# Optimization experiments

Measured on AMD Instinct MI355X. Metric: run time of the kernel, lower is better.

The kernel has to match this reference:

```python
import jax, jax.numpy as jnp
import numpy as np
from jax import lax

B, T, V, LAT, U, P = 256, 128, 42, 200, 512, 3  # batch, seq, vocab, latent, lstm units, num_prop


def setup_inputs() -> dict:
    key = jax.random.key(0)
    ks = jax.random.split(key, 40)
    g = lambda i, shape, s=0.05: (jax.random.normal(ks[i], shape, jnp.float32) * s)
    inp = {
        'X': jax.random.randint(ks[0], (B, T), 0, V, jnp.int64 if jax.config.jax_enable_x64 else jnp.int32),
        'Y': jax.random.randint(ks[1], (B, T), 0, V, jnp.int32),
        'C': jax.random.normal(ks[2], (B, P), jnp.float32),
        'L': jax.random.randint(ks[3], (B,), 1, T + 1, jnp.int32),
        'eps': jax.random.normal(ks[4], (B, LAT), jnp.float32),
        'emb_enc': g(5, (V, LAT), 0.1),
        'emb_dec': g(6, (V, LAT), 0.1),
        # encoder stacked LSTM: layer0 input dim = LAT + P, layers 1-2 input dim = U
        'enc_k0': g(7, (LAT + P, 4 * U)), 'enc_rk0': g(8, (U, 4 * U)), 'enc_b0': jnp.zeros((4 * U,), jnp.float32),
        'enc_k1': g(9, (U, 4 * U)), 'enc_rk1': g(10, (U, 4 * U)), 'enc_b1': jnp.zeros((4 * U,), jnp.float32),
        'enc_k2': g(11, (U, 4 * U)), 'enc_rk2': g(12, (U, 4 * U)), 'enc_b2': jnp.zeros((4 * U,), jnp.float32),
        # decoder stacked LSTM: layer0 input dim = 2*LAT + P
        'dec_k0': g(13, (2 * LAT + P, 4 * U)), 'dec_rk0': g(14, (U, 4 * U)), 'dec_b0': jnp.zeros((4 * U,), jnp.float32),
        'dec_k1': g(15, (U, 4 * U)), 'dec_rk1': g(16, (U, 4 * U)), 'dec_b1': jnp.zeros((4 * U,), jnp.float32),
        'dec_k2': g(17, (U, 4 * U)), 'dec_rk2': g(18, (U, 4 * U)), 'dec_b2': jnp.zeros((4 * U,), jnp.float32),
        'Wm': g(19, (U, LAT)), 'bm': jnp.zeros((LAT,), jnp.float32),
        'Ws': g(20, (U, LAT)), 'bs': jnp.zeros((LAT,), jnp.float32),
        'Wo': g(21, (U, V)), 'bo': jnp.zeros((V,), jnp.float32),
    }
    return inp


def _lstm_step(x, h, c, k, rk, b):
    # Keras LSTMCell gate order: i, f, g(candidate), o
    z = x @ k + h @ rk + b
    i, f, gg, o = jnp.split(z, 4, axis=-1)
    c2 = jax.nn.sigmoid(f) * c + jax.nn.sigmoid(i) * jnp.tanh(gg)
    h2 = jax.nn.sigmoid(o) * jnp.tanh(c2)
    return h2, c2


def _run_stacked(inp, params):
    # inp: [B, T, D]; params: list of 3 (kernel, recurrent_kernel, bias)
    b = inp.shape[0]
    init = tuple((jnp.zeros((b, U), inp.dtype), jnp.zeros((b, U), inp.dtype)) for _ in range(3))

    def scan_fn(carry, x_t):
        h_in = x_t
        new = []
        for (h, c), (k, rk, bb) in zip(carry, params):
            h2, c2 = _lstm_step(h_in, h, c, k, rk, bb)
            new.append((h2, c2))
            h_in = h2
        return tuple(new), h_in

    carry, ys = lax.scan(scan_fn, init, jnp.swapaxes(inp, 0, 1))
    return jnp.swapaxes(ys, 0, 1), carry  # [B,T,U], final states


def reference(X, Y, C, L, eps, emb_enc, emb_dec,
              enc_k0, enc_rk0, enc_b0, enc_k1, enc_rk1, enc_b1, enc_k2, enc_rk2, enc_b2,
              dec_k0, dec_rk0, dec_b0, dec_k1, dec_rk1, dec_b1, dec_k2, dec_rk2, dec_b2,
              Wm, bm, Ws, bs, Wo, bo):
    enc_params = [(enc_k0, enc_rk0, enc_b0), (enc_k1, enc_rk1, enc_b1), (enc_k2, enc_rk2, enc_b2)]
    dec_params = [(dec_k0, dec_rk0, dec_b0), (dec_k1, dec_rk1, dec_b1), (dec_k2, dec_rk2, dec_b2)]

    # ---- encode ----
    Xe = emb_enc[X]                                       # [B,T,LAT]
    Ct = jnp.broadcast_to(C[:, None, :], (B, T, P))
    enc_in = jnp.concatenate([Xe, Ct], axis=-1)           # [B,T,LAT+P]
    _, enc_states = _run_stacked(enc_in, enc_params)
    h = enc_states[-1][1]                                 # CELL state of last layer (state[-1][1])
    mean = h @ Wm + bm
    log_sigma = h @ Ws + bs
    z = mean + jnp.exp(log_sigma / 2.0) * eps             # [B,LAT]

    # ---- decode ----
    Zt = jnp.broadcast_to(z[:, None, :], (B, T, LAT))
    Xd = emb_dec[X]
    dec_in = jnp.concatenate([Zt, Xd, Ct], axis=-1)       # [B,T,2*LAT+P]
    dec_out, _ = _run_stacked(dec_in, dec_params)
    pre = dec_out @ Wo + bo                               # pre-softmax logits [B,T,V]

    # ---- losses ----
    logp = jax.nn.log_softmax(pre, axis=-1)
    ce = -jnp.take_along_axis(logp, Y[..., None].astype(jnp.int32), axis=-1)[..., 0]  # [B,T]
    weights = (jnp.arange(T)[None, :] < L[:, None]).astype(jnp.float32)
    recon = jnp.mean(ce * weights)
    latent = -0.5 * jnp.mean(1.0 + log_sigma - jnp.square(mean) - jnp.exp(log_sigma))
    loss = recon + latent
    return loss, recon, latent
```

## Files before the change

### kernel.cpp

```cpp
#include <hip/hip_runtime.h>

#define B_ 256
#define T_ 128
#define V_ 42
#define LAT_ 200
#define U_ 512
#define G4_ 2048
#define NBLK 196
#define FI(r, m) ((((r) * 2) + (m)) * 32)
#define SLOT_ ((size_t)B_ * U_)
#define LS_ ((size_t)129 * SLOT_)

typedef unsigned short ushort_t;
typedef __attribute__((ext_vector_type(8))) short bf8;
typedef __attribute__((ext_vector_type(4))) float f4;

__device__ __forceinline__ ushort_t f2bf(float f) {
  union { float f; unsigned int i; } v; v.f = f;
  unsigned int r = v.i + 0x7fffu + ((v.i >> 16) & 1u);
  return (ushort_t)(r >> 16);
}
__device__ __forceinline__ float sigf(float x) { return 1.f / (1.f + __expf(-x)); }
__device__ __forceinline__ float tanhfast(float x) {
  float e = __expf(2.f * x);
  return 1.f - 2.f / (e + 1.f);
}
__device__ __forceinline__ void wait_vm0() {
  asm volatile("s_waitcnt vmcnt(0)" ::: "memory");
}
__device__ __forceinline__ void st_wt_b16(void* p, ushort_t v) {
  unsigned int vv = v;
  asm volatile("global_store_short %0, %1, off sc0 sc1" :: "v"(p), "v"(vv) : "memory");
}
__device__ __forceinline__ void st_wt_b32(void* p, unsigned int v) {
  asm volatile("global_store_dword %0, %1, off sc0 sc1" :: "v"(p), "v"(v) : "memory");
}

__global__ __launch_bounds__(256) void table_kernel(const float* emb, const float* k0, int roff, float* table) {
  int v = blockIdx.x, tid = threadIdx.x;
  __shared__ float e[LAT_];
  for (int i = tid; i < LAT_; i += 256) e[i] = emb[v * LAT_ + i];
  __syncthreads();
  for (int j = tid; j < G4_; j += 256) {
    float s = 0.f;
    for (int n = 0; n < LAT_; n++) s += e[n] * k0[(size_t)(roff + n) * G4_ + j];
    table[v * G4_ + j] = s;
  }
}

__device__ __forceinline__ size_t mat_off_u4(int m) {
  if (m == 0) return 0;
  if (m == 1) return 147456;
  if (m < 10) return 360448 + (size_t)(m - 2) * 131072;
  return 1409024;
}

struct SwzSrc {
  const float *enc_rk0, *enc_k0, *enc_b0;
  const float *dec_rk0, *dec_k0, *dec_b0;
  const float *tabE, *tabD;
  const float *encK1, *encR1, *encK2, *encR2;
  const float *decK1, *decR1, *decK2, *decR2;
  const float *Wo;
  ushort_t* dst;
};

__device__ float swz_val(const SwzSrc& s, int mat, int k, int n) {
  switch (mat) {
    case 0: {
      if (k < 512) return s.enc_rk0[(size_t)k * G4_ + n];
      int i = k - 512;
      if (i < 42) return s.tabE[(size_t)i * G4_ + n];
      if (i < 45) return s.enc_k0[(size_t)(200 + i - 42) * G4_ + n];
      if (i == 45) return s.enc_b0[n];
      return 0.f;
    }
    case 1: {
      if (k < 512) return s.dec_rk0[(size_t)k * G4_ + n];
      int i = k - 512;
      if (i < 200) return s.dec_k0[(size_t)i * G4_ + n];
      if (i < 256) return 0.f;
      i -= 256;
      if (i < 42) return s.tabD[(size_t)i * G4_ + n];
      if (i < 45) return s.dec_k0[(size_t)(400 + i - 42) * G4_ + n];
      if (i == 45) return s.dec_b0[n];
      return 0.f;
    }
    case 2: return s.encK1[(size_t)k * G4_ + n];
    case 3: return s.encR1[(size_t)k * G4_ + n];
    case 4: return s.encK2[(size_t)k * G4_ + n];
    case 5: return s.encR2[(size_t)k * G4_ + n];
    case 6: return s.decK1[(size_t)k * G4_ + n];
    case 7: return s.decR1[(size_t)k * G4_ + n];
    case 8: return s.decK2[(size_t)k * G4_ + n];
    case 9: return s.decR2[(size_t)k * G4_ + n];
    default: return (n < V_) ? s.Wo[(size_t)k * V_ + n] : 0.f;
  }
}

__global__ __launch_bounds__(256) void swz_ext_kernel(SwzSrc s) {
  int b = blockIdx.x, tid = threadIdx.x;
  int mat, nt16;
  if (b < 1280) { mat = b >> 7; nt16 = b & 127; } else { mat = 10; nt16 = b - 1280; }
  int ktMax = (mat == 0) ? 18 : (mat == 1) ? 26 : 16;
  int lane = tid & 63, l15 = lane & 15, q = lane >> 4;
  int n = nt16 * 16 + l15;
  uint4* dst = (uint4*)s.dst;
  size_t off = mat_off_u4(mat);
  for (int kt = tid >> 6; kt < ktMax; kt += 4) {
    ushort_t o[8];
    int kb = kt * 32 + q * 8;
#pragma unroll
    for (int j = 0; j < 8; j++) o[j] = f2bf(swz_val(s, mat, kb + j, n));
    dst[off + ((size_t)nt16 * ktMax + kt) * 64 + lane] = *(const uint4*)o;
  }
}

struct PP {
  const ushort_t* swz;
  ushort_t* ring;
  float* c2g; ushort_t* zf16; float* sums; int* bar; int* gen; int* flg; float* out;
  const float *enc_b1, *enc_b2, *dec_b1, *dec_b2;
  const float *Wm, *bm, *Ws, *bs, *eps, *C, *bo;
  const int *X, *Y, *Lb;
};

__device__ __forceinline__ void grid_barrier(int* bar, int* gen) {
  __builtin_amdgcn_fence(__ATOMIC_RELEASE, "agent");
  __syncthreads();
  if (threadIdx.x == 0) {
    int g = __hip_atomic_load(gen, __ATOMIC_RELAXED, __HIP_MEMORY_SCOPE_AGENT);
    if (__hip_atomic_fetch_add(bar, 1, __ATOMIC_ACQ_REL, __HIP_MEMORY_SCOPE_AGENT) == NBLK - 1) {
      __hip_atomic_store(bar, 0, __ATOMIC_RELAXED, __HIP_MEMORY_SCOPE_AGENT);
      __hip_atomic_store(gen, g + 1, __ATOMIC_RELEASE, __HIP_MEMORY_SCOPE_AGENT);
    } else {
      int gg;
      do {
        __builtin_amdgcn_s_sleep(1);
        gg = __hip_atomic_load(gen, __ATOMIC_ACQUIRE, __HIP_MEMORY_SCOPE_AGENT);
      } while (gg == g);
    }
  }
  __syncthreads();
  __builtin_amdgcn_fence(__ATOMIC_ACQUIRE, "agent");
}

#define MFMA(a, bfrag, c) __builtin_amdgcn_mfma_f32_16x16x32_bf16((a), (bfrag), (c), 0, 0, 0)

__device__ __forceinline__ void wait_flags(const int* f, int cnt, int target, f4* junk, bf8 ja) {
  int lane = threadIdx.x & 63;
  const int* a = f + (lane < cnt ? lane : 0);
  for (;;) {
    int v = __hip_atomic_load(a, __ATOMIC_RELAXED, __HIP_MEMORY_SCOPE_AGENT);
    bool bad = (lane < cnt) && (v < target);
    if (__ballot(bad) == 0ull) return;
#pragma unroll
    for (int i = 0; i < 8; i++) *junk = MFMA(ja, ja, *junk);
  }
}

__global__ __launch_bounds__(256, 1) void persist(PP p) {
  __shared__ uint4 wlds4[8192];
  const int b = blockIdx.x, tid = threadIdx.x;
  const int lane = tid & 63, w = tid >> 6, q = lane >> 4, l15 = lane & 15;
  const int role = b < 64 ? 0 : b < 128 ? 1 : b < 192 ? 2 : 3;
  const int idx = b & 63;
  const int ut = idx >> 1;
  const int mi = idx & 1;
  const int m0 = mi * 128;
  const int rw = m0 + w * 32;
  const int u = ut * 16 + l15;
  const uint4* swzU4 = (const uint4*)p.swz;
  const int cb = b - 192;

  unsigned char* tok = (unsigned char*)wlds4 + 106496;
  unsigned char* ytok = (unsigned char*)wlds4 + 49152;

  f4 junk = {0.f, 0.f, 0.f, 0.f};
  bf8 ja = {0, 0, 0, 0, 0, 0, 0, 0};

  ushort_t cb0[2][3];
  if (role == 0) {
#pragma unroll
    for (int ms = 0; ms < 2; ms++)
#pragma unroll
      for (int j = 0; j < 3; j++) cb0[ms][j] = f2bf(p.C[(rw + ms * 16 + l15) * 3 + j]);
  }

  const int pubidx = FI(role, mi) + ut;

  float ce_local = 0.f;
  float boR0 = 0.f, boR1 = 0.f, boR2 = 0.f;
  int Lr[4] = {0, 0, 0, 0};
  int pub = 0;

  for (int phase = 0; phase < 2; phase++) {
    const bool dec = (phase == 1);

    if (dec) {
      grid_barrier(p.bar, p.gen);
      if (b < 50) {
        int lat0 = b * 4;
        int row = tid;
        float m[4], ls[4];
#pragma unroll
        for (int lc = 0; lc < 4; lc++) { m[lc] = p.bm[lat0 + lc]; ls[lc] = p.bs[lat0 + lc]; }
        const float* cr = p.c2g + (size_t)row * U_;
        for (int k = 0; k < U_; k++) {
          float hv = cr[k];
#pragma unroll
          for (int lc = 0; lc < 4; lc++) {
            m[lc] += hv * p.Wm[k * LAT_ + lat0 + lc];
            ls[lc] += hv * p.Ws[k * LAT_ + lat0 + lc];
          }
        }
        float kl = 0.f;
#pragma unroll
        for (int lc = 0; lc < 4; lc++) {
          int lat = lat0 + lc;
          float zz = m[lc] + __expf(0.5f * ls[lc]) * p.eps[row * LAT_ + lat];
          p.zf16[row * 256 + lat] = f2bf(zz);
          kl += 1.f + ls[lc] - m[lc] * m[lc] - __expf(ls[lc]);
        }
        float* red = (float*)wlds4;
        red[tid] = kl; __syncthreads();
        for (int st = 128; st > 0; st >>= 1) { if (tid < st) red[tid] += red[tid + st]; __syncthreads(); }
        if (tid == 0) atomicAdd(p.sums + 1, red[0]);
      }
      __syncthreads();
    }

    if (role == 0) {
      if (!dec) {
        size_t mo = mat_off_u4(0);
        for (int g = 0; g < 4; g++) {
          int nt16 = g * 32 + ut;
          size_t src = mo + (size_t)nt16 * 18 * 64;
          int dst = g * 18 * 64;
          for (int i = tid; i < 18 * 64; i += 256) wlds4[dst + i] = swzU4[src + i];
        }
        for (int i = tid; i < 128 * T_; i += 256) {
          int r = i >> 7, t = i & 127;
          tok[r * 133 + t] = (unsigned char)p.X[(size_t)(m0 + r) * T_ + t];
        }
      } else {
        size_t mo = mat_off_u4(1);
        for (int g = 0; g < 4; g++) {
          int nt16 = g * 32 + ut;
          size_t src = mo + (size_t)nt16 * 26 * 64;
          int dst = g * 18 * 64;
          for (int i = tid; i < 16 * 64; i += 256) wlds4[dst + i] = swzU4[src + i];
          for (int i = tid; i < 2 * 64; i += 256) wlds4[dst + 16 * 64 + i] = swzU4[src + 24 * 64 + i];
          for (int i = tid; i < 8 * 64; i += 256) wlds4[4608 + g * 512 + i] = swzU4[src + 16 * 64 + i];
        }
      }
    } else if (role <= 2) {
      int matK = dec ? (role == 1 ? 6 : 8) : (role == 1 ? 2 : 4);
      for (int gm = 0; gm < 2; gm++) {
        size_t mo = mat_off_u4(matK + gm);
        for (int g = 0; g < 4; g++) {
          int nt16 = g * 32 + ut;
          size_t src = mo + (size_t)nt16 * 1024;
          int dst = gm * 4096 + g * 1024;
          for (int i = tid; i < 1024; i += 256) wlds4[dst + i] = swzU4[src + i];
        }
      }
    } else if (dec) {
      size_t mo = mat_off_u4(10);
      for (int i = tid; i < 3072; i += 256) wlds4[i] = swzU4[mo + i];
      for (int i = tid; i < 64 * T_; i += 256) {
        int r = i >> 7, t = i & 127;
        ytok[r * 133 + t] = (unsigned char)p.Y[(size_t)(cb * 64 + r) * T_ + t];
      }
      int r0c = cb * 64 + w * 16;
      boR0 = p.bo[l15]; boR1 = p.bo[16 + l15]; boR2 = (l15 < 10) ? p.bo[32 + l15] : 0.f;
#pragma unroll
      for (int r = 0; r < 4; r++) Lr[r] = p.Lb[r0c + q * 4 + r];
    }
    __syncthreads();

    float creg[2][4];
#pragma unroll
    for (int ms = 0; ms < 2; ms++)
#pragma unroll
      for (int r = 0; r < 4; r++) creg[ms][r] = 0.f;
    float bias[4] = {0.f, 0.f, 0.f, 0.f};
    if (role == 1 || role == 2) {
      const float* bb = dec ? (role == 1 ? p.dec_b1 : p.dec_b2) : (role == 1 ? p.enc_b1 : p.enc_b2);
#pragma unroll
      for (int g = 0; g < 4; g++) bias[g] = bb[g * 512 + u];
    }

    const int* myp = nullptr; int myc = 0;
    if (role == 0) {
      if (w == 0) { myp = p.flg + FI(0, mi); myc = 32; }
    } else if (role == 1) {
      if (w == 0) { myp = p.flg + FI(0, mi); myc = 32; }
      else if (w == 1) { myp = p.flg + FI(1, mi); myc = 32; }
    } else if (role == 2) {
      if (w == 0) { myp = p.flg + FI(1, mi); myc = 32; }
      else if (w == 1) { myp = p.flg + FI(2, mi); myc = 32; }
    } else {
      if (w == 0) { myp = p.flg + FI(2, cb >> 1); myc = 32; }
    }

    grid_barrier(p.bar, p.gen);

    f4 zacc[2][4];
#pragma unroll
    for (int ms = 0; ms < 2; ms++)
#pragma unroll
      for (int g = 0; g < 4; g++) zacc[ms][g] = (f4){0.f, 0.f, 0.f, 0.f};
    if (role == 0 && dec) {
      const ushort_t* Az0 = p.zf16 + (rw + l15) * 256 + q * 8;
#pragma unroll
      for (int kz = 0; kz < 8; kz++) {
        bf8 a0 = *(const bf8*)(Az0 + kz * 32);
        bf8 a1 = *(const bf8*)(Az0 + 16 * 256 + kz * 32);
#pragma unroll
        for (int g = 0; g < 4; g++) {
          bf8 bbf = *(const bf8*)&wlds4[4608 + g * 512 + kz * 64 + lane];
          zacc[0][g] = MFMA(a0, bbf, zacc[0][g]);
          zacc[1][g] = MFMA(a1, bbf, zacc[1][g]);
        }
      }
    }

    const int smax = dec ? T_ + 3 : T_ + 2;
    for (int s = 0; s < smax; s++) {
      pub++;
      if (myc) wait_flags(myp, myc, pub - 1, &junk, ja);
      __syncthreads();

      const int lag = (role <= 2) ? role : 3;
      const int t = s - lag;
      if (role == 3) {
        if (dec && t >= 0 && t < T_) {
          int r0c = cb * 64 + w * 16;
          const ushort_t* Ar = p.ring + 2 * LS_ + (size_t)(t + 1) * SLOT_ + (size_t)(r0c + l15) * U_ + q * 8;
          f4 a3[3];
#pragma unroll
          for (int nt = 0; nt < 3; nt++) a3[nt] = (f4){0.f, 0.f, 0.f, 0.f};
#pragma unroll 4
          for (int kt = 0; kt < 16; kt++) {
            bf8 a = *(const bf8*)(Ar + kt * 32);
#pragma unroll
            for (int nt = 0; nt < 3; nt++) {
              bf8 bbf = *(const bf8*)&wlds4[nt * 1024 + kt * 64 + lane];
              a3[nt] = MFMA(a, bbf, a3[nt]);
            }
          }
#pragma unroll
          for (int r = 0; r < 4; r++) {
            float v0 = a3[0][r] + boR0;
            float v1 = a3[1][r] + boR1;
            float v2 = (l15 < 10) ? a3[2][r] + boR2 : -3.0e38f;
            float mx = fmaxf(fmaxf(v0, v1), v2);
            mx = fmaxf(mx, __shfl_xor(mx, 1)); mx = fmaxf(mx, __shfl_xor(mx, 2));
            mx = fmaxf(mx, __shfl_xor(mx, 4)); mx = fmaxf(mx, __shfl_xor(mx, 8));
            float se = __expf(v0 - mx) + __expf(v1 - mx) + ((l15 < 10) ? __expf(v2 - mx) : 0.f);
            int yv = ytok[(w * 16 + q * 4 + r) * 133 + t];
            float py = (l15 == yv ? v0 : 0.f) + (l15 + 16 == yv ? v1 : 0.f) + (l15 + 32 == yv ? v2 : 0.f);
            se += __shfl_xor(se, 1); se += __shfl_xor(se, 2); se += __shfl_xor(se, 4); se += __shfl_xor(se, 8);
            py += __shfl_xor(py, 1); py += __shfl_xor(py, 2); py += __shfl_xor(py, 4); py += __shfl_xor(py, 8);
            if (l15 == 0 && t < Lr[r]) ce_local += mx + __logf(se) - py;
          }
        }
      } else if (t >= 0 && t < T_) {
        f4 acc[2][4];
#pragma unroll
        for (int ms = 0; ms < 2; ms++)
#pragma unroll
          for (int g = 0; g < 4; g++) acc[ms][g] = zacc[ms][g];

        const ushort_t* hin = p.ring + (size_t)role * LS_ + (size_t)t * SLOT_;
        ushort_t* hout = p.ring + (size_t)role * LS_ + (size_t)(t + 1) * SLOT_;
        const ushort_t* Ah0 = hin + (size_t)(rw + l15) * U_ + q * 8;
        const ushort_t* Ah1 = Ah0 + 16 * U_;

        if (role == 0) {
          const int KT64 = 18 * 64;
#pragma unroll 4
          for (int kt = 0; kt < 16; kt++) {
            bf8 a0 = *(const bf8*)(Ah0 + kt * 32);
            bf8 a1 = *(const bf8*)(Ah1 + kt * 32);
#pragma unroll
            for (int g = 0; g < 4; g++) {
              bf8 bbf = *(const bf8*)&wlds4[g * KT64 + kt * 64 + lane];
              acc[0][g] = MFMA(a0, bbf, acc[0][g]);
              acc[1][g] = MFMA(a1, bbf, acc[1][g]);
            }
          }
          int xv0 = tok[(w * 32 + l15) * 133 + t];
          int xv1 = tok[(w * 32 + 16 + l15) * 133 + t];
#pragma unroll
          for (int ktc = 0; ktc < 2; ktc++) {
            union { ushort_t us[8]; bf8 v; } a0u, a1u;
#pragma unroll
            for (int j = 0; j < 8; j++) {
              int id = ktc * 32 + q * 8 + j;
              ushort_t v0 = (id == xv0) ? (ushort_t)0x3F80 : (ushort_t)0;
              ushort_t v1 = (id == xv1) ? (ushort_t)0x3F80 : (ushort_t)0;
              if (id >= 42 && id < 45) { v0 = cb0[0][id - 42]; v1 = cb0[1][id - 42]; }
              if (id == 45) { v0 = 0x3F80; v1 = 0x3F80; }
              a0u.us[j] = v0; a1u.us[j] = v1;
            }
            int kt = 16 + ktc;
#pragma unroll
            for (int g = 0; g < 4; g++) {
              bf8 bbf = *(const bf8*)&wlds4[g * KT64 + kt * 64 + lane];
              acc[0][g] = MFMA(a0u.v, bbf, acc[0][g]);
              acc[1][g] = MFMA(a1u.v, bbf, acc[1][g]);
            }
          }
        } else {
          const ushort_t* xin = p.ring + (size_t)(role - 1) * LS_ + (size_t)(t + 1) * SLOT_;
          const ushort_t* Ax0 = xin + (size_t)(rw + l15) * U_ + q * 8;
          const ushort_t* Ax1 = Ax0 + 16 * U_;
#pragma unroll 4
          for (int kt = 0; kt < 16; kt++) {
            bf8 a0 = *(const bf8*)(Ax0 + kt * 32);
            bf8 a1 = *(const bf8*)(Ax1 + kt * 32);
#pragma unroll
            for (int g = 0; g < 4; g++) {
              bf8 bbf = *(const bf8*)&wlds4[g * 1024 + kt * 64 + lane];
              acc[0][g] = MFMA(a0, bbf, acc[0][g]);
              acc[1][g] = MFMA(a1, bbf, acc[1][g]);
            }
          }
#pragma unroll 4
          for (int kt = 0; kt < 16; kt++) {
            bf8 a0 = *(const bf8*)(Ah0 + kt * 32);
            bf8 a1 = *(const bf8*)(Ah1 + kt * 32);
#pragma unroll
            for (int g = 0; g < 4; g++) {
              bf8 bbf = *(const bf8*)&wlds4[4096 + g * 1024 + kt * 64 + lane];
              acc[0][g] = MFMA(a0, bbf, acc[0][g]);
              acc[1][g] = MFMA(a1, bbf, acc[1][g]);
            }
          }
        }

#pragma unroll
        for (int ms = 0; ms < 2; ms++)
#pragma unroll
          for (int r = 0; r < 4; r++) {
            int row = rw + ms * 16 + q * 4 + r;
            float zi = acc[ms][0][r] + bias[0];
            float zf = acc[ms][1][r] + bias[1];
            float zg = acc[ms][2][r] + bias[2];
            float zo = acc[ms][3][r] + bias[3];
            float cp = creg[ms][r];
            float cn = sigf(zf) * cp + sigf(zi) * tanhfast(zg);
            float hn = sigf(zo) * tanhfast(cn);
            creg[ms][r] = cn;
            st_wt_b16(&hout[(size_t)row * U_ + u], f2bf(hn));
            if (!dec && role == 2 && t == T_ - 1) p.c2g[(size_t)row * U_ + u] = cn;
          }
      }
      wait_vm0();
      __syncthreads();
      if (tid == 0 && role < 3) st_wt_b32(p.flg + pubidx, (unsigned int)pub);
    }
  }

  if (p.X[0] == 0x12345678 && tid == 0) atomicAdd(p.out, junk[0]);

  if (role == 3 && l15 == 0) atomicAdd(p.sums + 0, ce_local);
  grid_barrier(p.bar, p.gen);
  if (b == 0 && tid == 0) {
    float recon = p.sums[0] * (1.f / ((float)B_ * (float)T_));
    float latent = -0.5f * p.sums[1] * (1.f / ((float)B_ * (float)LAT_));
    p.out[0] = recon + latent;
    p.out[1] = recon;
    p.out[2] = latent;
  }
}

extern "C" void kernel_launch(void* const* d_in, const int* in_sizes, int n_in,
                              void* d_out, int out_size, void* d_ws, size_t ws_size,
                              hipStream_t stream) {
  const int*   X       = (const int*)d_in[0];
  const int*   Y       = (const int*)d_in[1];
  const float* C       = (const float*)d_in[2];
  const int*   L       = (const int*)d_in[3];
  const float* eps     = (const float*)d_in[4];
  const float* emb_enc = (const float*)d_in[5];
  const float* emb_dec = (const float*)d_in[6];
  const float* enc_k0  = (const float*)d_in[7];
  const float* enc_rk0 = (const float*)d_in[8];
  const float* enc_b0  = (const float*)d_in[9];
  const float* enc_k1  = (const float*)d_in[10];
  const float* enc_rk1 = (const float*)d_in[11];
  const float* enc_b1  = (const float*)d_in[12];
  const float* enc_k2  = (const float*)d_in[13];
  const float* enc_rk2 = (const float*)d_in[14];
  const float* enc_b2  = (const float*)d_in[15];
  const float* dec_k0  = (const float*)d_in[16];
  const float* dec_rk0 = (const float*)d_in[17];
  const float* dec_b0  = (const float*)d_in[18];
  const float* dec_k1  = (const float*)d_in[19];
  const float* dec_rk1 = (const float*)d_in[20];
  const float* dec_b1  = (const float*)d_in[21];
  const float* dec_k2  = (const float*)d_in[22];
  const float* dec_rk2 = (const float*)d_in[23];
  const float* dec_b2  = (const float*)d_in[24];
  const float* Wm      = (const float*)d_in[25];
  const float* bm      = (const float*)d_in[26];
  const float* Ws      = (const float*)d_in[27];
  const float* bs      = (const float*)d_in[28];
  const float* Wo      = (const float*)d_in[29];
  const float* bo      = (const float*)d_in[30];
  float* out = (float*)d_out;
  (void)in_sizes; (void)n_in; (void)out_size; (void)ws_size;

  char* wsb = (char*)d_ws;
  size_t o = 0;
  auto take = [&](size_t bytes) -> char* { char* p = wsb + o; o += (bytes + 255) & ~(size_t)255; return p; };

  float* c2g  = (float*)take((size_t)B_ * U_ * 4);
  ushort_t* zf16 = (ushort_t*)take((size_t)B_ * 256 * 2);
  float* sums = (float*)take(8);
  int* bar = (int*)take(4);
  int* gen = (int*)take(4);
  int* flg = (int*)take(4 * 2 * 32 * 4);
  size_t zero_bytes = o;
  ushort_t* ring = (ushort_t*)take(3 * LS_ * 2);
  ushort_t* swz = (ushort_t*)take((size_t)1412096 * 16);
  float* tabE = (float*)take((size_t)V_ * G4_ * 4);
  float* tabD = (float*)take((size_t)V_ * G4_ * 4);

  hipMemsetAsync(wsb, 0, zero_bytes, stream);
  for (int l = 0; l < 3; l++)
    hipMemsetAsync(ring + (size_t)l * LS_, 0, SLOT_ * 2, stream);

  table_kernel<<<V_, 256, 0, stream>>>(emb_enc, enc_k0, 0, tabE);
  table_kernel<<<V_, 256, 0, stream>>>(emb_dec, dec_k0, 200, tabD);

  SwzSrc ss;
  ss.enc_rk0 = enc_rk0; ss.enc_k0 = enc_k0; ss.enc_b0 = enc_b0;
  ss.dec_rk0 = dec_rk0; ss.dec_k0 = dec_k0; ss.dec_b0 = dec_b0;
  ss.tabE = tabE; ss.tabD = tabD;
  ss.encK1 = enc_k1; ss.encR1 = enc_rk1; ss.encK2 = enc_k2; ss.encR2 = enc_rk2;
  ss.decK1 = dec_k1; ss.decR1 = dec_rk1; ss.decK2 = dec_k2; ss.decR2 = dec_rk2;
  ss.Wo = Wo; ss.dst = swz;
  swz_ext_kernel<<<1283, 256, 0, stream>>>(ss);

  PP pp;
  pp.swz = swz; pp.ring = ring;
  pp.c2g = c2g; pp.zf16 = zf16; pp.sums = sums; pp.bar = bar; pp.gen = gen; pp.flg = flg; pp.out = out;
  pp.enc_b1 = enc_b1; pp.enc_b2 = enc_b2; pp.dec_b1 = dec_b1; pp.dec_b2 = dec_b2;
  pp.Wm = Wm; pp.bm = bm; pp.Ws = Ws; pp.bs = bs; pp.eps = eps; pp.C = C; pp.bo = bo;
  pp.X = X; pp.Y = Y; pp.Lb = L;
  persist<<<NBLK, 256, 0, stream>>>(pp);
}
```

Baseline: 4.997 ms.

## Pack h stores into 64-bit writes and add MFMA busy-work to hold clocks

Each LSTM hidden-state output was written as a separate 16-bit write-through store. Lanes now exchange bf16 values through two xor shuffles so that one lane in four issues a single 8-byte write-through store, cutting the store count on the critical cross-block handoff. The flag-wait loop and the end of each step now run dummy MFMA chains across four independent accumulators, apparently to keep the matrix units busy and the clocks high while spinning. The dummy work costs power and adds latency to every step, and its effect depends on the device's clock behaviour.

Result: slower. 6.057 ms (+21.2%).

```diff
diff --git a/kernel.cpp b/kernel.cpp
--- a/kernel.cpp
+++ b/kernel.cpp
@@ -28,12 +28,11 @@
 __device__ __forceinline__ void wait_vm0() {
   asm volatile("s_waitcnt vmcnt(0)" ::: "memory");
 }
-__device__ __forceinline__ void st_wt_b16(void* p, ushort_t v) {
-  unsigned int vv = v;
-  asm volatile("global_store_short %0, %1, off sc0 sc1" :: "v"(p), "v"(vv) : "memory");
-}
 __device__ __forceinline__ void st_wt_b32(void* p, unsigned int v) {
   asm volatile("global_store_dword %0, %1, off sc0 sc1" :: "v"(p), "v"(v) : "memory");
+}
+__device__ __forceinline__ void st_wt_b64(void* p, unsigned long long v) {
+  asm volatile("global_store_dwordx2 %0, %1, off sc0 sc1" :: "v"(p), "v"(v) : "memory");
 }
 
 __global__ __launch_bounds__(256) void table_kernel(const float* emb, const float* k0, int roff, float* table) {
@@ -147,15 +146,19 @@
 
 #define MFMA(a, bfrag, c) __builtin_amdgcn_mfma_f32_16x16x32_bf16((a), (bfrag), (c), 0, 0, 0)
 
-__device__ __forceinline__ void wait_flags(const int* f, int cnt, int target, f4* junk, bf8 ja) {
+__device__ __forceinline__ void wait_flags(const int* f, int cnt, int target, f4* jk, bf8 ja) {
   int lane = threadIdx.x & 63;
   const int* a = f + (lane < cnt ? lane : 0);
+  int burn = 0;
   for (;;) {
     int v = __hip_atomic_load(a, __ATOMIC_RELAXED, __HIP_MEMORY_SCOPE_AGENT);
+    for (int i = 0; i < burn; i++) {
+      jk[0] = MFMA(ja, ja, jk[0]); jk[1] = MFMA(ja, ja, jk[1]);
+      jk[2] = MFMA(ja, ja, jk[2]); jk[3] = MFMA(ja, ja, jk[3]);
+    }
     bool bad = (lane < cnt) && (v < target);
     if (__ballot(bad) == 0ull) return;
-#pragma unroll
-    for (int i = 0; i < 8; i++) *junk = MFMA(ja, ja, *junk);
+    burn = 32;
   }
 }
 
@@ -176,7 +179,7 @@
   unsigned char* tok = (unsigned char*)wlds4 + 106496;
   unsigned char* ytok = (unsigned char*)wlds4 + 49152;
 
-  f4 junk = {0.f, 0.f, 0.f, 0.f};
+  f4 junk[4] = {{0.f,0.f,0.f,0.f},{0.f,0.f,0.f,0.f},{0.f,0.f,0.f,0.f},{0.f,0.f,0.f,0.f}};
   bf8 ja = {0, 0, 0, 0, 0, 0, 0, 0};
 
   ushort_t cb0[2][3];
@@ -329,7 +332,7 @@
     const int smax = dec ? T_ + 3 : T_ + 2;
     for (int s = 0; s < smax; s++) {
       pub++;
-      if (myc) wait_flags(myp, myc, pub - 1, &junk, ja);
+      if (myc) wait_flags(myp, myc, pub - 1, junk, ja);
       __syncthreads();
 
       const int lag = (role <= 2) ? role : 3;
@@ -454,9 +457,22 @@
             float cn = sigf(zf) * cp + sigf(zi) * tanhfast(zg);
             float hn = sigf(zo) * tanhfast(cn);
             creg[ms][r] = cn;
-            st_wt_b16(&hout[(size_t)row * U_ + u], f2bf(hn));
+            unsigned int v0 = (unsigned int)f2bf(hn);
+            unsigned int pr = (unsigned int)__shfl_xor((int)v0, 1);
+            unsigned int p2 = (l15 & 1) ? ((pr & 0xffffu) | (v0 << 16))
+                                        : ((v0 & 0xffffu) | (pr << 16));
+            unsigned int pr2 = (unsigned int)__shfl_xor((int)p2, 2);
+            unsigned long long p4 = (l15 & 2)
+              ? (((unsigned long long)pr2) | (((unsigned long long)p2) << 32))
+              : (((unsigned long long)p2) | (((unsigned long long)pr2) << 32));
+            if ((l15 & 3) == 0)
+              st_wt_b64(&hout[(size_t)row * U_ + ut * 16 + (l15 & 12)], p4);
             if (!dec && role == 2 && t == T_ - 1) p.c2g[(size_t)row * U_ + u] = cn;
           }
+      }
+      for (int i = 0; i < 16; i++) {
+        junk[0] = MFMA(ja, ja, junk[0]); junk[1] = MFMA(ja, ja, junk[1]);
+        junk[2] = MFMA(ja, ja, junk[2]); junk[3] = MFMA(ja, ja, junk[3]);
       }
       wait_vm0();
       __syncthreads();
@@ -464,7 +480,8 @@
     }
   }
 
-  if (p.X[0] == 0x12345678 && tid == 0) atomicAdd(p.out, junk[0]);
+  if (p.X[0] == 0x12345678 && tid == 0)
+    atomicAdd(p.out, junk[0][0] + junk[1][0] + junk[2][0] + junk[3][0]);
 
   if (role == 3 && l15 == 0) atomicAdd(p.sums + 0, ce_local);
   grid_barrier(p.bar, p.gen);
```

## Prefetch layer inputs one step ahead and remap blocks across 256 CUs

Applied to the files above, without the earlier changes.

Blocks are remapped so roles interleave across the grid (grp = b&7), and the grid grows to 256 blocks, with extra idle/projection blocks. Layers 1–2 and the output head now load next step's input activations into registers (xpre/arpre) after computing the current step, waiting on the upstream flag early, and the pipeline lag doubles to allow this. The MFMA-spinning junk loop in wait_flags is removed. This trades register pressure and more pipeline stages for hiding global-load latency behind the recurrence.

New measurement: 9.215 ms. +84.4%, slower.

```diff
diff --git a/kernel.cpp b/kernel.cpp
--- a/kernel.cpp
+++ b/kernel.cpp
@@ -6,7 +6,7 @@
 #define LAT_ 200
 #define U_ 512
 #define G4_ 2048
-#define NBLK 196
+#define NBLK 256
 #define FI(r, m) ((((r) * 2) + (m)) * 32)
 #define SLOT_ ((size_t)B_ * U_)
 #define LS_ ((size_t)129 * SLOT_)
@@ -145,39 +145,36 @@
   __builtin_amdgcn_fence(__ATOMIC_ACQUIRE, "agent");
 }
 
-#define MFMA(a, bfrag, c) __builtin_amdgcn_mfma_f32_16x16x32_bf16((a), (bfrag), (c), 0, 0, 0)
-
-__device__ __forceinline__ void wait_flags(const int* f, int cnt, int target, f4* junk, bf8 ja) {
+__device__ __forceinline__ void wait_flags(const int* f, int cnt, int target) {
   int lane = threadIdx.x & 63;
   const int* a = f + (lane < cnt ? lane : 0);
-  for (;;) {
+  bool bad;
+  do {
     int v = __hip_atomic_load(a, __ATOMIC_RELAXED, __HIP_MEMORY_SCOPE_AGENT);
-    bool bad = (lane < cnt) && (v < target);
-    if (__ballot(bad) == 0ull) return;
-#pragma unroll
-    for (int i = 0; i < 8; i++) *junk = MFMA(ja, ja, *junk);
-  }
-}
+    bad = (lane < cnt) && (v < target);
+  } while (__ballot(bad) != 0ull);
+}
+
+#define MFMA(a, bfrag, c) __builtin_amdgcn_mfma_f32_16x16x32_bf16((a), (bfrag), (c), 0, 0, 0)
 
 __global__ __launch_bounds__(256, 1) void persist(PP p) {
   __shared__ uint4 wlds4[8192];
   const int b = blockIdx.x, tid = threadIdx.x;
   const int lane = tid & 63, w = tid >> 6, q = lane >> 4, l15 = lane & 15;
-  const int role = b < 64 ? 0 : b < 128 ? 1 : b < 192 ? 2 : 3;
-  const int idx = b & 63;
-  const int ut = idx >> 1;
-  const int mi = idx & 1;
+
+  const int grp = b & 7, rank = b >> 3;
+  int role, mi = 0, cb = 0, pid = -1;
+  if (grp < 6) { role = grp >> 1; mi = grp & 1; }
+  else if (grp == 6 && rank < 4) { role = 3; cb = rank; mi = rank >> 1; }
+  else { role = 4; pid = (grp == 6) ? rank - 4 : 28 + rank; }
+  const int ut = rank;
   const int m0 = mi * 128;
   const int rw = m0 + w * 32;
   const int u = ut * 16 + l15;
   const uint4* swzU4 = (const uint4*)p.swz;
-  const int cb = b - 192;
 
   unsigned char* tok = (unsigned char*)wlds4 + 106496;
   unsigned char* ytok = (unsigned char*)wlds4 + 49152;
-
-  f4 junk = {0.f, 0.f, 0.f, 0.f};
-  bf8 ja = {0, 0, 0, 0, 0, 0, 0, 0};
 
   ushort_t cb0[2][3];
   if (role == 0) {
@@ -192,15 +189,15 @@
   float ce_local = 0.f;
   float boR0 = 0.f, boR1 = 0.f, boR2 = 0.f;
   int Lr[4] = {0, 0, 0, 0};
-  int pub = 0;
 
   for (int phase = 0; phase < 2; phase++) {
     const bool dec = (phase == 1);
+    const int base = dec ? (T_ + 4) : 0;
 
     if (dec) {
       grid_barrier(p.bar, p.gen);
-      if (b < 50) {
-        int lat0 = b * 4;
+      if (pid >= 0 && pid < 50) {
+        int lat0 = pid * 4;
         int row = tid;
         float m[4], ls[4];
 #pragma unroll
@@ -265,7 +262,7 @@
           for (int i = tid; i < 1024; i += 256) wlds4[dst + i] = swzU4[src + i];
         }
       }
-    } else if (dec) {
+    } else if (role == 3 && dec) {
       size_t mo = mat_off_u4(10);
       for (int i = tid; i < 3072; i += 256) wlds4[i] = swzU4[mo + i];
       for (int i = tid; i < 64 * T_; i += 256) {
@@ -291,19 +288,6 @@
       for (int g = 0; g < 4; g++) bias[g] = bb[g * 512 + u];
     }
 
-    const int* myp = nullptr; int myc = 0;
-    if (role == 0) {
-      if (w == 0) { myp = p.flg + FI(0, mi); myc = 32; }
-    } else if (role == 1) {
-      if (w == 0) { myp = p.flg + FI(0, mi); myc = 32; }
-      else if (w == 1) { myp = p.flg + FI(1, mi); myc = 32; }
-    } else if (role == 2) {
-      if (w == 0) { myp = p.flg + FI(1, mi); myc = 32; }
-      else if (w == 1) { myp = p.flg + FI(2, mi); myc = 32; }
-    } else {
-      if (w == 0) { myp = p.flg + FI(2, cb >> 1); myc = 32; }
-    }
-
     grid_barrier(p.bar, p.gen);
 
     f4 zacc[2][4];
@@ -326,145 +310,162 @@
       }
     }
 
-    const int smax = dec ? T_ + 3 : T_ + 2;
-    for (int s = 0; s < smax; s++) {
-      pub++;
-      if (myc) wait_flags(myp, myc, pub - 1, &junk, ja);
-      __syncthreads();
-
-      const int lag = (role <= 2) ? role : 3;
-      const int t = s - lag;
-      if (role == 3) {
-        if (dec && t >= 0 && t < T_) {
+    const bool active = (role < 3) || (role == 3 && dec);
+    if (active) {
+      const int lag = (role <= 2) ? 2 * role : 6;
+      const int smax = dec ? T_ + 6 : T_ + 4;
+      bf8 xpre[2][16];
+      bf8 arpre[16];
+      for (int s = 0; s < smax; s++) {
+        const int pubv = base + s + 1;
+        if (role < 3 && w == 0) wait_flags(p.flg + FI(role, mi), 32, pubv - 1);
+        __syncthreads();
+
+        const int t = s - lag;
+        if (role == 3) {
+          if (t >= 0 && t < T_) {
+            f4 a3[3];
+#pragma unroll
+            for (int nt = 0; nt < 3; nt++) a3[nt] = (f4){0.f, 0.f, 0.f, 0.f};
+#pragma unroll
+            for (int kt = 0; kt < 16; kt++) {
+#pragma unroll
+              for (int nt = 0; nt < 3; nt++) {
+                bf8 bbf = *(const bf8*)&wlds4[nt * 1024 + kt * 64 + lane];
+                a3[nt] = MFMA(arpre[kt], bbf, a3[nt]);
+              }
+            }
+#pragma unroll
+            for (int r = 0; r < 4; r++) {
+              float v0 = a3[0][r] + boR0;
+              float v1 = a3[1][r] + boR1;
+              float v2 = (l15 < 10) ? a3[2][r] + boR2 : -3.0e38f;
+              float mx = fmaxf(fmaxf(v0, v1), v2);
+              mx = fmaxf(mx, __shfl_xor(mx, 1)); mx = fmaxf(mx, __shfl_xor(mx, 2));
+              mx = fmaxf(mx, __shfl_xor(mx, 4)); mx = fmaxf(mx, __shfl_xor(mx, 8));
+              float se = __expf(v0 - mx) + __expf(v1 - mx) + ((l15 < 10) ? __expf(v2 - mx) : 0.f);
+              int yv = ytok[(w * 16 + q * 4 + r) * 133 + t];
+              float py = (l15 == yv ? v0 : 0.f) + (l15 + 16 == yv ? v1 : 0.f) + (l15 + 32 == yv ? v2 : 0.f);
+              se += __shfl_xor(se, 1); se += __shfl_xor(se, 2); se += __shfl_xor(se, 4); se += __shfl_xor(se, 8);
+              py += __shfl_xor(py, 1); py += __shfl_xor(py, 2); py += __shfl_xor(py, 4); py += __shfl_xor(py, 8);
+              if (l15 == 0 && t < Lr[r]) ce_local += mx + __logf(se) - py;
+            }
+          }
+        } else if (t >= 0 && t < T_) {
+          f4 acc[2][4];
+#pragma unroll
+          for (int ms = 0; ms < 2; ms++)
+#pragma unroll
+            for (int g = 0; g < 4; g++) acc[ms][g] = zacc[ms][g];
+
+          const ushort_t* hin = p.ring + (size_t)role * LS_ + (size_t)t * SLOT_;
+          ushort_t* hout = p.ring + (size_t)role * LS_ + (size_t)(t + 1) * SLOT_;
+          const ushort_t* Ah0 = hin + (size_t)(rw + l15) * U_ + q * 8;
+          const ushort_t* Ah1 = Ah0 + 16 * U_;
+
+          if (role == 0) {
+            const int KT64 = 18 * 64;
+#pragma unroll 4
+            for (int kt = 0; kt < 16; kt++) {
+              bf8 a0 = *(const bf8*)(Ah0 + kt * 32);
+              bf8 a1 = *(const bf8*)(Ah1 + kt * 32);
+#pragma unroll
+              for (int g = 0; g < 4; g++) {
+                bf8 bbf = *(const bf8*)&wlds4[g * KT64 + kt * 64 + lane];
+                acc[0][g] = MFMA(a0, bbf, acc[0][g]);
+                acc[1][g] = MFMA(a1, bbf, acc[1][g]);
+              }
+            }
+            int xv0 = tok[(w * 32 + l15) * 133 + t];
+            int xv1 = tok[(w * 32 + 16 + l15) * 133 + t];
+#pragma unroll
+            for (int ktc = 0; ktc < 2; ktc++) {
+              union { ushort_t us[8]; bf8 v; } a0u, a1u;
+#pragma unroll
+              for (int j = 0; j < 8; j++) {
+                int id = ktc * 32 + q * 8 + j;
+                ushort_t v0 = (id == xv0) ? (ushort_t)0x3F80 : (ushort_t)0;
+                ushort_t v1 = (id == xv1) ? (ushort_t)0x3F80 : (ushort_t)0;
+                if (id >= 42 && id < 45) { v0 = cb0[0][id - 42]; v1 = cb0[1][id - 42]; }
+                if (id == 45) { v0 = 0x3F80; v1 = 0x3F80; }
+                a0u.us[j] = v0; a1u.us[j] = v1;
+              }
+              int kt = 16 + ktc;
+#pragma unroll
+              for (int g = 0; g < 4; g++) {
+                bf8 bbf = *(const bf8*)&wlds4[g * KT64 + kt * 64 + lane];
+                acc[0][g] = MFMA(a0u.v, bbf, acc[0][g]);
+                acc[1][g] = MFMA(a1u.v, bbf, acc[1][g]);
+              }
+            }
+          } else {
+#pragma unroll
+            for (int kt = 0; kt < 16; kt++) {
+#pragma unroll
+              for (int g = 0; g < 4; g++) {
+                bf8 bbf = *(const bf8*)&wlds4[g * 1024 + kt * 64 + lane];
+                acc[0][g] = MFMA(xpre[0][kt], bbf, acc[0][g]);
+                acc[1][g] = MFMA(xpre[1][kt], bbf, acc[1][g]);
+              }
+            }
+#pragma unroll 4
+            for (int kt = 0; kt < 16; kt++) {
+              bf8 a0 = *(const bf8*)(Ah0 + kt * 32);
+              bf8 a1 = *(const bf8*)(Ah1 + kt * 32);
+#pragma unroll
+              for (int g = 0; g < 4; g++) {
+                bf8 bbf = *(const bf8*)&wlds4[4096 + g * 1024 + kt * 64 + lane];
+                acc[0][g] = MFMA(a0, bbf, acc[0][g]);
+                acc[1][g] = MFMA(a1, bbf, acc[1][g]);
+              }
+            }
+          }
+
+#pragma unroll
+          for (int ms = 0; ms < 2; ms++)
+#pragma unroll
+            for (int r = 0; r < 4; r++) {
+              int row = rw + ms * 16 + q * 4 + r;
+              float zi = acc[ms][0][r] + bias[0];
+              float zf = acc[ms][1][r] + bias[1];
+              float zg = acc[ms][2][r] + bias[2];
+              float zo = acc[ms][3][r] + bias[3];
+              float cp = creg[ms][r];
+              float cn = sigf(zf) * cp + sigf(zi) * tanhfast(zg);
+              float hn = sigf(zo) * tanhfast(cn);
+              creg[ms][r] = cn;
+              ushort_t hv = f2bf(hn);
+              ushort_t* addr = &hout[(size_t)row * U_ + u];
+              *addr = hv;
+              st_wt_b16(addr, hv);
+              if (!dec && role == 2 && t == T_ - 1) p.c2g[(size_t)row * U_ + u] = cn;
+            }
+        }
+
+        const int tn = s + 1 - lag;
+        if ((role == 1 || role == 2) && tn >= 0 && tn < T_) {
+          wait_flags(p.flg + FI(role - 1, mi), 32, pubv - 1);
+          const ushort_t* xin = p.ring + (size_t)(role - 1) * LS_ + (size_t)(tn + 1) * SLOT_;
+          const ushort_t* Ax0 = xin + (size_t)(rw + l15) * U_ + q * 8;
+#pragma unroll
+          for (int kt = 0; kt < 16; kt++) {
+            xpre[0][kt] = *(const bf8*)(Ax0 + kt * 32);
+            xpre[1][kt] = *(const bf8*)(Ax0 + 16 * U_ + kt * 32);
+          }
+        } else if (role == 3 && tn >= 0 && tn < T_) {
+          wait_flags(p.flg + FI(2, cb >> 1), 32, pubv - 1);
           int r0c = cb * 64 + w * 16;
-          const ushort_t* Ar = p.ring + 2 * LS_ + (size_t)(t + 1) * SLOT_ + (size_t)(r0c + l15) * U_ + q * 8;
-          f4 a3[3];
-#pragma unroll
-          for (int nt = 0; nt < 3; nt++) a3[nt] = (f4){0.f, 0.f, 0.f, 0.f};
-#pragma unroll 4
-          for (int kt = 0; kt < 16; kt++) {
-            bf8 a = *(const bf8*)(Ar + kt * 32);
-#pragma unroll
-            for (int nt = 0; nt < 3; nt++) {
-              bf8 bbf = *(const bf8*)&wlds4[nt * 1024 + kt * 64 + lane];
-              a3[nt] = MFMA(a, bbf, a3[nt]);
-            }
-          }
-#pragma unroll
-          for (int r = 0; r < 4; r++) {
-            float v0 = a3[0][r] + boR0;
-            float v1 = a3[1][r] + boR1;
-            float v2 = (l15 < 10) ? a3[2][r] + boR2 : -3.0e38f;
-            float mx = fmaxf(fmaxf(v0, v1), v2);
-            mx = fmaxf(mx, __shfl_xor(mx, 1)); mx = fmaxf(mx, __shfl_xor(mx, 2));
-            mx = fmaxf(mx, __shfl_xor(mx, 4)); mx = fmaxf(mx, __shfl_xor(mx, 8));
-            float se = __expf(v0 - mx) + __expf(v1 - mx) + ((l15 < 10) ? __expf(v2 - mx) : 0.f);
-            int yv = ytok[(w * 16 + q * 4 + r) * 133 + t];
-            float py = (l15 == yv ? v0 : 0.f) + (l15 + 16 == yv ? v1 : 0.f) + (l15 + 32 == yv ? v2 : 0.f);
-            se += __shfl_xor(se, 1); se += __shfl_xor(se, 2); se += __shfl_xor(se, 4); se += __shfl_xor(se, 8);
-            py += __shfl_xor(py, 1); py += __shfl_xor(py, 2); py += __shfl_xor(py, 4); py += __shfl_xor(py, 8);
-            if (l15 == 0 && t < Lr[r]) ce_local += mx + __logf(se) - py;
-          }
-        }
-      } else if (t >= 0 && t < T_) {
-        f4 acc[2][4];
-#pragma unroll
-        for (int ms = 0; ms < 2; ms++)
-#pragma unroll
-          for (int g = 0; g < 4; g++) acc[ms][g] = zacc[ms][g];
-
-        const ushort_t* hin = p.ring + (size_t)role * LS_ + (size_t)t * SLOT_;
-        ushort_t* hout = p.ring + (size_t)role * LS_ + (size_t)(t + 1) * SLOT_;
-        const ushort_t* Ah0 = hin + (size_t)(rw + l15) * U_ + q * 8;
-        const ushort_t* Ah1 = Ah0 + 16 * U_;
-
-        if (role == 0) {
-          const int KT64 = 18 * 64;
-#pragma unroll 4
-          for (int kt = 0; kt < 16; kt++) {
-            bf8 a0 = *(const bf8*)(Ah0 + kt * 32);
-            bf8 a1 = *(const bf8*)(Ah1 + kt * 32);
-#pragma unroll
-            for (int g = 0; g < 4; g++) {
-              bf8 bbf = *(const bf8*)&wlds4[g * KT64 + kt * 64 + lane];
-              acc[0][g] = MFMA(a0, bbf, acc[0][g]);
-              acc[1][g] = MFMA(a1, bbf, acc[1][g]);
-            }
-          }
-          int xv0 = tok[(w * 32 + l15) * 133 + t];
-          int xv1 = tok[(w * 32 + 16 + l15) * 133 + t];
-#pragma unroll
-          for (int ktc = 0; ktc < 2; ktc++) {
-            union { ushort_t us[8]; bf8 v; } a0u, a1u;
-#pragma unroll
-            for (int j = 0; j < 8; j++) {
-              int id = ktc * 32 + q * 8 + j;
-              ushort_t v0 = (id == xv0) ? (ushort_t)0x3F80 : (ushort_t)0;
-              ushort_t v1 = (id == xv1) ? (ushort_t)0x3F80 : (ushort_t)0;
-              if (id >= 42 && id < 45) { v0 = cb0[0][id - 42]; v1 = cb0[1][id - 42]; }
-              if (id == 45) { v0 = 0x3F80; v1 = 0x3F80; }
-              a0u.us[j] = v0; a1u.us[j] = v1;
-            }
-            int kt = 16 + ktc;
-#pragma unroll
-            for (int g = 0; g < 4; g++) {
-              bf8 bbf = *(const bf8*)&wlds4[g * KT64 + kt * 64 + lane];
-              acc[0][g] = MFMA(a0u.v, bbf, acc[0][g]);
-              acc[1][g] = MFMA(a1u.v, bbf, acc[1][g]);
-            }
-          }
-        } else {
-          const ushort_t* xin = p.ring + (size_t)(role - 1) * LS_ + (size_t)(t + 1) * SLOT_;
-          const ushort_t* Ax0 = xin + (size_t)(rw + l15) * U_ + q * 8;
-          const ushort_t* Ax1 = Ax0 + 16 * U_;
-#pragma unroll 4
-          for (int kt = 0; kt < 16; kt++) {
-            bf8 a0 = *(const bf8*)(Ax0 + kt * 32);
-            bf8 a1 = *(const bf8*)(Ax1 + kt * 32);
-#pragma unroll
-            for (int g = 0; g < 4; g++) {
-              bf8 bbf = *(const bf8*)&wlds4[g * 1024 + kt * 64 + lane];
-              acc[0][g] = MFMA(a0, bbf, acc[0][g]);
-              acc[1][g] = MFMA(a1, bbf, acc[1][g]);
-            }
-          }
-#pragma unroll 4
-          for (int kt = 0; kt < 16; kt++) {
-            bf8 a0 = *(const bf8*)(Ah0 + kt * 32);
-            bf8 a1 = *(const bf8*)(Ah1 + kt * 32);
-#pragma unroll
-            for (int g = 0; g < 4; g++) {
-              bf8 bbf = *(const bf8*)&wlds4[4096 + g * 1024 + kt * 64 + lane];
-              acc[0][g] = MFMA(a0, bbf, acc[0][g]);
-              acc[1][g] = MFMA(a1, bbf, acc[1][g]);
-            }
-          }
-        }
-
-#pragma unroll
-        for (int ms = 0; ms < 2; ms++)
-#pragma unroll
-          for (int r = 0; r < 4; r++) {
-            int row = rw + ms * 16 + q * 4 + r;
-            float zi = acc[ms][0][r] + bias[0];
-            float zf = acc[ms][1][r] + bias[1];
-            float zg = acc[ms][2][r] + bias[2];
-            float zo = acc[ms][3][r] + bias[3];
-            float cp = creg[ms][r];
-            float cn = sigf(zf) * cp + sigf(zi) * tanhfast(zg);
-            float hn = sigf(zo) * tanhfast(cn);
-            creg[ms][r] = cn;
-            st_wt_b16(&hout[(size_t)row * U_ + u], f2bf(hn));
-            if (!dec && role == 2 && t == T_ - 1) p.c2g[(size_t)row * U_ + u] = cn;
-          }
+          const ushort_t* Ar = p.ring + 2 * LS_ + (size_t)(tn + 1) * SLOT_ + (size_t)(r0c + l15) * U_ + q * 8;
+#pragma unroll
+          for (int kt = 0; kt < 16; kt++) arpre[kt] = *(const bf8*)(Ar + kt * 32);
+        }
+
+        wait_vm0();
+        __syncthreads();
+        if (tid == 0 && role < 3) st_wt_b32(p.flg + pubidx, (unsigned int)pubv);
       }
-      wait_vm0();
-      __syncthreads();
-      if (tid == 0 && role < 3) st_wt_b32(p.flg + pubidx, (unsigned int)pub);
-    }
-  }
-
-  if (p.X[0] == 0x12345678 && tid == 0) atomicAdd(p.out, junk[0]);
+    }
+  }
 
   if (role == 3 && l15 == 0) atomicAdd(p.sums + 0, ce_local);
   grid_barrier(p.bar, p.gen);
```
